# Performance work log

Hardware: AMD Instinct MI355X
Metric: run time of the kernel (lower is better)

## Reference

```python
import jax, jax.numpy as jnp
import numpy as np
import math

B, S, D, H, L, DFF, V = 4, 1024, 512, 8, 4, 2048, 32000
DK = D // H
SPARSITY = 0.3
K = max(1, int(S * SPARSITY))  # 307
EPS = 1e-5


def _layernorm(x, g, b):
    mu = jnp.mean(x, axis=-1, keepdims=True)
    var = jnp.mean(jnp.square(x - mu), axis=-1, keepdims=True)
    return (x - mu) * jax.lax.rsqrt(var + EPS) * g + b


def _scatter_topk(scores, k):
    # scores: [B,H,S,S]. keep top-k per row, others -inf (torch.topk + scatter_)
    vals, idx = jax.lax.top_k(scores, k)
    lead = int(np.prod(scores.shape[:-1]))
    sk = scores.shape[-1]
    sparse = jnp.full((lead, sk), -jnp.inf, dtype=scores.dtype)
    rows = jnp.arange(lead)[:, None]
    sparse = sparse.at[rows, idx.reshape(lead, k)].set(vals.reshape(lead, k))
    return sparse.reshape(scores.shape)


def _forward(x, tok_emb, pos_emb, Wq, bq, Wk, bk, Wv, bv, Wo, bo,
             g1, be1, g2, be2, W1, b1, Wm, bm, W2, b2, Wout, bout):
    h = tok_emb[x] + pos_emb[jnp.arange(S)][None, :, :]  # [B,S,D]
    scale = 1.0 / math.sqrt(DK)
    for l in range(L):
        y = _layernorm(h, g1[l], be1[l])
        q = (y @ Wq[l] + bq[l]).reshape(B, S, H, DK).transpose(0, 2, 1, 3)
        kk = (y @ Wk[l] + bk[l]).reshape(B, S, H, DK).transpose(0, 2, 1, 3)
        v = (y @ Wv[l] + bv[l]).reshape(B, S, H, DK).transpose(0, 2, 1, 3)
        scores = jnp.einsum('bhqd,bhkd->bhqk', q, kk) * scale
        sparse = _scatter_topk(scores, K)
        attn = jax.nn.softmax(sparse, axis=-1)
        o = jnp.einsum('bhqk,bhkd->bhqd', attn, v)
        o = o.transpose(0, 2, 1, 3).reshape(B, S, D) @ Wo[l] + bo[l]
        h = h + o
        z = _layernorm(h, g2[l], be2[l])
        f = jax.nn.gelu(z @ W1[l] + b1[l], approximate=False)
        f = jax.nn.gelu(f @ Wm[l] + bm[l], approximate=False)
        f = f @ W2[l] + b2[l]
        h = h + f
    return h @ Wout + bout  # logits [B,S,V]


def setup_inputs() -> dict:
    key = jax.random.key(0)
    ks = iter(jax.random.split(key, 32))
    xa = lambda shape, fan: (jax.random.normal(next(ks), shape, jnp.float32)
                             * math.sqrt(2.0 / fan))
    return {
        'x': jax.random.randint(next(ks), (B, S), 0, V, dtype=jnp.int32),
        'tok_emb': xa((V, D), V + D),
        'pos_emb': xa((S, D), S + D),
        'Wq': xa((L, D, D), 2 * D), 'bq': jnp.zeros((L, D), jnp.float32),
        'Wk': xa((L, D, D), 2 * D), 'bk': jnp.zeros((L, D), jnp.float32),
        'Wv': xa((L, D, D), 2 * D), 'bv': jnp.zeros((L, D), jnp.float32),
        'Wo': xa((L, D, D), 2 * D), 'bo': jnp.zeros((L, D), jnp.float32),
        'g1': jnp.ones((L, D), jnp.float32), 'be1': jnp.zeros((L, D), jnp.float32),
        'g2': jnp.ones((L, D), jnp.float32), 'be2': jnp.zeros((L, D), jnp.float32),
        'W1': xa((L, D, DFF), D + DFF), 'b1': jnp.zeros((L, DFF), jnp.float32),
        'Wm': xa((L, DFF, DFF), 2 * DFF), 'bm': jnp.zeros((L, DFF), jnp.float32),
        'W2': xa((L, DFF, D), D + DFF), 'b2': jnp.zeros((L, D), jnp.float32),
        'Wout': xa((D, V), D + V), 'bout': jnp.zeros((V,), jnp.float32),
    }


def reference(x, tok_emb, pos_emb, Wq, bq, Wk, bk, Wv, bv, Wo, bo,
              g1, be1, g2, be2, W1, b1, Wm, bm, W2, b2, Wout, bout):
    return _forward(x, tok_emb, pos_emb, Wq, bq, Wk, bk, Wv, bv, Wo, bo,
                    g1, be1, g2, be2, W1, b1, Wm, bm, W2, b2, Wout, bout)
```

## Files before the change

### kernel.cpp

```cpp
#include <hip/hip_runtime.h>
#include <hip/hip_bf16.h>
#include <math.h>

#define B_ 4
#define S_ 1024
#define D_ 512
#define H_ 8
#define L_ 4
#define DFF_ 2048
#define V_ 32000
#define DK_ 64
#define KTOP 307
#define SRS 1048

using bf16x8 = __attribute__((ext_vector_type(8))) __bf16;
using bf16x4 = __attribute__((ext_vector_type(4))) __bf16;
using bf16x2 = __attribute__((ext_vector_type(2))) __bf16;
using f32x4v = __attribute__((ext_vector_type(4))) float;

__device__ __forceinline__ void gload_lds16(const __bf16* g, __bf16* l) {
  __builtin_amdgcn_global_load_lds(
      (const __attribute__((address_space(1))) void*)g,
      (__attribute__((address_space(3))) void*)l, 16, 0, 0);
}

__device__ __forceinline__ unsigned int f32_to_bf16_bits(float s) {
  unsigned int x = __float_as_uint(s);
  return (x + 0x7FFFu + ((x >> 16) & 1u)) >> 16;
}

__global__ void embed_kernel(const int* __restrict__ x, const float* __restrict__ tok,
                             const float* __restrict__ pos, float* __restrict__ h) {
  int row = blockIdx.x;
  int t = threadIdx.x;
  int s = row & (S_ - 1);
  int token = x[row];
  const float4* t4 = reinterpret_cast<const float4*>(tok + (size_t)token * D_);
  const float4* p4 = reinterpret_cast<const float4*>(pos + (size_t)s * D_);
  float4 a = t4[t];
  float4 b = p4[t];
  a.x += b.x; a.y += b.y; a.z += b.z; a.w += b.w;
  reinterpret_cast<float4*>(h + (size_t)row * D_)[t] = a;
}

__global__ void ln_kernel(const float* __restrict__ xin, const float* __restrict__ g,
                          const float* __restrict__ bta, __bf16* __restrict__ y) {
  int row = blockIdx.x;
  int t = threadIdx.x;
  const float2* x2 = reinterpret_cast<const float2*>(xin + (size_t)row * D_);
  float2 v = x2[t];
  float s = v.x + v.y;
  #pragma unroll
  for (int m = 1; m < 64; m <<= 1) s += __shfl_xor(s, m, 64);
  __shared__ float red[4];
  __shared__ float red2[4];
  int wid = t >> 6, lane = t & 63;
  if (lane == 0) red[wid] = s;
  __syncthreads();
  float mu = (red[0] + red[1] + red[2] + red[3]) * (1.0f / D_);
  float dx = v.x - mu, dy = v.y - mu;
  float s2 = dx * dx + dy * dy;
  #pragma unroll
  for (int m = 1; m < 64; m <<= 1) s2 += __shfl_xor(s2, m, 64);
  if (lane == 0) red2[wid] = s2;
  __syncthreads();
  float var = (red2[0] + red2[1] + red2[2] + red2[3]) * (1.0f / D_);
  float rstd = rsqrtf(var + 1e-5f);
  float2 gg = reinterpret_cast<const float2*>(g)[t];
  float2 bb = reinterpret_cast<const float2*>(bta)[t];
  bf16x2 o2;
  o2[0] = (__bf16)(dx * rstd * gg.x + bb.x);
  o2[1] = (__bf16)(dy * rstd * gg.y + bb.y);
  *reinterpret_cast<bf16x2*>(y + (size_t)row * D_ + t * 2) = o2;
}

__global__ void transpose_bf16_kernel(const float* __restrict__ in, __bf16* __restrict__ out,
                                      int Kd, int N, long in_bstride, long out_bstride) {
  __shared__ float tile[32][33];
  const float* ib = in + (size_t)blockIdx.z * in_bstride;
  __bf16* ob = out + (size_t)blockIdx.z * out_bstride;
  int n0 = blockIdx.x * 32, k0 = blockIdx.y * 32;
  int tx = threadIdx.x & 31, ty = threadIdx.x >> 5;
  #pragma unroll
  for (int i = 0; i < 4; ++i)
    tile[ty + i * 8][tx] = ib[(size_t)(k0 + ty + i * 8) * N + n0 + tx];
  __syncthreads();
  #pragma unroll
  for (int i = 0; i < 4; ++i)
    ob[(size_t)(n0 + ty + i * 8) * Kd + k0 + tx] = (__bf16)tile[tx][ty + i * 8];
}

__global__ void concat_bias_kernel(const float* __restrict__ bq, const float* __restrict__ bk,
                                   const float* __restrict__ bv, float* __restrict__ bqkv) {
  int i = blockIdx.x * 256 + threadIdx.x;
  int l = i / 1536, c = i - l * 1536;
  float v = (c < 512) ? bq[l * 512 + c]
          : (c < 1024) ? bk[l * 512 + c - 512]
                       : bv[l * 512 + c - 1024];
  bqkv[i] = v;
}

#define BM 128
#define BN 128
#define BK 32

template<int OMODE, bool GELU_ACT, bool RES, bool SWZ>
__global__ __launch_bounds__(256)
void gemm_bf16_kernel(const __bf16* __restrict__ A, const __bf16* __restrict__ WT,
                      const float* __restrict__ bias, const float* __restrict__ res,
                      void* __restrict__ outp, void* __restrict__ outp2, void* __restrict__ outp3,
                      int M, int N, int Kd) {
  __shared__ __bf16 As[BM * BK];
  __shared__ __bf16 Ws[BN * BK];
  int tid = threadIdx.x;
  int lane = tid & 63, w = tid >> 6;
  int wr = w >> 1, wc = w & 1;
  int lr = lane & 15, lg = lane >> 4;
  int bx, by;
  if (SWZ) {
    int lid = blockIdx.x;
    int cpx = gridDim.x >> 3;
    int swz = (lid & 7) * cpx + (lid >> 3);
    int gx = M >> 7;
    bx = swz % gx;
    by = swz / gx;
  } else {
    bx = blockIdx.x; by = blockIdx.y;
  }
  int row0 = bx * BM, col0 = by * BN;

  int srow = lane >> 2;
  int schunk = lane & 3;
  const __bf16* Abase = A + (size_t)(row0 + srow) * Kd + schunk * 8;
  const __bf16* Wbase = WT + (size_t)(col0 + srow) * Kd + schunk * 8;

  f32x4v acc[4][4];
  #pragma unroll
  for (int i = 0; i < 4; ++i)
    #pragma unroll
    for (int j = 0; j < 4; ++j)
      #pragma unroll
      for (int e = 0; e < 4; ++e) acc[i][j][e] = 0.0f;

  for (int k0 = 0; k0 < Kd; k0 += BK) {
    #pragma unroll
    for (int p = 0; p < 2; ++p) {
      int r0 = p * 64 + w * 16;
      gload_lds16(Abase + (size_t)r0 * Kd + k0, &As[r0 * BK]);
      gload_lds16(Wbase + (size_t)r0 * Kd + k0, &Ws[r0 * BK]);
    }
    __syncthreads();
    bf16x8 af[4], bfr[4];
    #pragma unroll
    for (int mr = 0; mr < 4; ++mr)
      af[mr] = *reinterpret_cast<const bf16x8*>(&As[(wr * 64 + mr * 16 + lr) * BK + lg * 8]);
    #pragma unroll
    for (int nc = 0; nc < 4; ++nc)
      bfr[nc] = *reinterpret_cast<const bf16x8*>(&Ws[(wc * 64 + nc * 16 + lr) * BK + lg * 8]);
    #pragma unroll
    for (int mr = 0; mr < 4; ++mr)
      #pragma unroll
      for (int nc = 0; nc < 4; ++nc)
        acc[mr][nc] = __builtin_amdgcn_mfma_f32_16x16x32_bf16(af[mr], bfr[nc], acc[mr][nc], 0, 0, 0);
    __syncthreads();
  }

  #pragma unroll
  for (int mr = 0; mr < 4; ++mr) {
    #pragma unroll
    for (int nc = 0; nc < 4; ++nc) {
      int c = col0 + wc * 64 + nc * 16 + lr;
      int rb = row0 + wr * 64 + mr * 16 + lg * 4;
      float vv[4];
      #pragma unroll
      for (int j = 0; j < 4; ++j) {
        float t = acc[mr][nc][j] + bias[c];
        if (RES) t += res[(size_t)(rb + j) * N + c];
        if (GELU_ACT) t = 0.5f * t * (1.0f + erff(t * 0.70710678118654752f));
        vv[j] = t;
      }
      if (OMODE == 0) {
        float* out = (float*)outp;
        #pragma unroll
        for (int j = 0; j < 4; ++j) out[(size_t)(rb + j) * N + c] = vv[j];
      } else if (OMODE == 1) {
        __bf16* out = (__bf16*)outp;
        #pragma unroll
        for (int j = 0; j < 4; ++j) out[(size_t)(rb + j) * N + c] = (__bf16)vv[j];
      } else if (OMODE == 3) {
        float* out = (float*)outp;
        __bf16* out2 = (__bf16*)outp2;
        #pragma unroll
        for (int j = 0; j < 4; ++j) {
          out[(size_t)(rb + j) * N + c] = vv[j];
          out2[(size_t)(rb + j) * N + c] = (__bf16)vv[j];
        }
      } else {
        if (col0 < 512) {
          __bf16* out = (__bf16*)outp;
          #pragma unroll
          for (int j = 0; j < 4; ++j) out[(size_t)(rb + j) * D_ + c] = (__bf16)vv[j];
        } else if (col0 < 1024) {
          __bf16* out = (__bf16*)outp2;
          #pragma unroll
          for (int j = 0; j < 4; ++j) out[(size_t)(rb + j) * D_ + (c - 512)] = (__bf16)vv[j];
        } else {
          __bf16* out = (__bf16*)outp3;
          int b = rb >> 10, s0 = rb & (S_ - 1);
          bf16x4 pk;
          #pragma unroll
          for (int j = 0; j < 4; ++j) pk[j] = (__bf16)vv[j];
          *reinterpret_cast<bf16x4*>(&out[((size_t)b * D_ + (c - 1024)) * S_ + s0]) = pk;
        }
      }
    }
  }
}

template<int OMODE, bool RES>
__global__ __launch_bounds__(256)
void gemm64_kernel(const __bf16* __restrict__ A, const __bf16* __restrict__ WT,
                   const float* __restrict__ bias, const float* __restrict__ res,
                   void* __restrict__ outp, void* __restrict__ outp2,
                   int M, int N, int Kd) {
  __shared__ __bf16 As[64 * BK];
  __shared__ __bf16 Ws[BN * BK];
  int tid = threadIdx.x;
  int lane = tid & 63, w = tid >> 6;
  int wr = w >> 1, wc = w & 1;
  int lr = lane & 15, lg = lane >> 4;
  int row0 = blockIdx.x * 64, col0 = blockIdx.y * BN;

  int srow = lane >> 2;
  int schunk = lane & 3;
  const __bf16* Abase = A + (size_t)(row0 + srow) * Kd + schunk * 8;
  const __bf16* Wbase = WT + (size_t)(col0 + srow) * Kd + schunk * 8;

  f32x4v acc[2][4];
  #pragma unroll
  for (int i = 0; i < 2; ++i)
    #pragma unroll
    for (int j = 0; j < 4; ++j)
      #pragma unroll
      for (int e = 0; e < 4; ++e) acc[i][j][e] = 0.0f;

  for (int k0 = 0; k0 < Kd; k0 += BK) {
    gload_lds16(Abase + (size_t)(w * 16) * Kd + k0, &As[w * 16 * BK]);
    #pragma unroll
    for (int p = 0; p < 2; ++p) {
      int r0 = p * 64 + w * 16;
      gload_lds16(Wbase + (size_t)r0 * Kd + k0, &Ws[r0 * BK]);
    }
    __syncthreads();
    bf16x8 af[2], bfr[4];
    #pragma unroll
    for (int mr = 0; mr < 2; ++mr)
      af[mr] = *reinterpret_cast<const bf16x8*>(&As[(wr * 32 + mr * 16 + lr) * BK + lg * 8]);
    #pragma unroll
    for (int nc = 0; nc < 4; ++nc)
      bfr[nc] = *reinterpret_cast<const bf16x8*>(&Ws[(wc * 64 + nc * 16 + lr) * BK + lg * 8]);
    #pragma unroll
    for (int mr = 0; mr < 2; ++mr)
      #pragma unroll
      for (int nc = 0; nc < 4; ++nc)
        acc[mr][nc] = __builtin_amdgcn_mfma_f32_16x16x32_bf16(af[mr], bfr[nc], acc[mr][nc], 0, 0, 0);
    __syncthreads();
  }

  #pragma unroll
  for (int mr = 0; mr < 2; ++mr) {
    #pragma unroll
    for (int nc = 0; nc < 4; ++nc) {
      int c = col0 + wc * 64 + nc * 16 + lr;
      int rb = row0 + wr * 32 + mr * 16 + lg * 4;
      float vv[4];
      #pragma unroll
      for (int j = 0; j < 4; ++j) {
        float t = acc[mr][nc][j] + bias[c];
        if (RES) t += res[(size_t)(rb + j) * N + c];
        vv[j] = t;
      }
      if (OMODE == 0) {
        float* out = (float*)outp;
        #pragma unroll
        for (int j = 0; j < 4; ++j) out[(size_t)(rb + j) * N + c] = vv[j];
      } else {
        float* out = (float*)outp;
        __bf16* out2 = (__bf16*)outp2;
        #pragma unroll
        for (int j = 0; j < 4; ++j) {
          out[(size_t)(rb + j) * N + c] = vv[j];
          out2[(size_t)(rb + j) * N + c] = (__bf16)vv[j];
        }
      }
    }
  }
}

__global__ __launch_bounds__(256)
void attn_kernel(const __bf16* __restrict__ qm, const __bf16* __restrict__ km,
                 const __bf16* __restrict__ vt, __bf16* __restrict__ o) {
  __shared__ unsigned short sc16[16][SRS];
  __shared__ float rs[16];
  const int q0 = blockIdx.x * 16;
  const int hh = blockIdx.y;
  const int bb = blockIdx.z;
  const int tid = threadIdx.x;
  const int lane = tid & 63, w = tid >> 6;
  const int lr = lane & 15, lg = lane >> 4;

  const __bf16* qrow = qm + ((size_t)(bb * S_ + q0 + lr)) * D_ + hh * DK_;
  bf16x8 qf0 = *reinterpret_cast<const bf16x8*>(qrow + lg * 8);
  bf16x8 qf1 = *reinterpret_cast<const bf16x8*>(qrow + 32 + lg * 8);

  const __bf16* kbase = km + ((size_t)bb * S_) * D_ + hh * DK_;
  #pragma unroll 4
  for (int kt = 0; kt < 16; ++kt) {
    int key0 = kt * 64 + w * 16;
    const __bf16* krow = kbase + (size_t)(key0 + lr) * D_;
    bf16x8 kf0 = *reinterpret_cast<const bf16x8*>(krow + lg * 8);
    bf16x8 kf1 = *reinterpret_cast<const bf16x8*>(krow + 32 + lg * 8);
    f32x4v d = {0.0f, 0.0f, 0.0f, 0.0f};
    d = __builtin_amdgcn_mfma_f32_16x16x32_bf16(qf0, kf0, d, 0, 0, 0);
    d = __builtin_amdgcn_mfma_f32_16x16x32_bf16(qf1, kf1, d, 0, 0, 0);
    #pragma unroll
    for (int j = 0; j < 4; ++j) {
      unsigned int u = f32_to_bf16_bits(d[j] * 0.125f);
      u = (u & 0x8000u) ? (~u & 0xFFFFu) : (u | 0x8000u);
      sc16[lg * 4 + j][key0 + lr] = (unsigned short)u;
    }
  }
  __syncthreads();

  {
    int r = tid >> 4, tc = tid & 15;
    const unsigned int* srow = reinterpret_cast<const unsigned int*>(&sc16[r][0]);
    unsigned int wv[32];
    #pragma unroll
    for (int g = 0; g < 8; ++g) {
      uint4 t4 = *reinterpret_cast<const uint4*>(&srow[g * 64 + tc * 4]);
      wv[g * 4 + 0] = t4.x; wv[g * 4 + 1] = t4.y;
      wv[g * 4 + 2] = t4.z; wv[g * 4 + 3] = t4.w;
    }
    unsigned int umax = 0;
    #pragma unroll
    for (int i = 0; i < 32; ++i) {
      unsigned int a = wv[i] & 0xFFFFu, b = wv[i] >> 16;
      unsigned int mx = a > b ? a : b;
      umax = mx > umax ? mx : umax;
    }
    #pragma unroll
    for (int m = 1; m < 16; m <<= 1) {
      unsigned int other = (unsigned int)__shfl_xor((int)umax, m, 64);
      umax = other > umax ? other : umax;
    }
    unsigned int lo = 0;
    for (int bit = 15; bit >= 0; --bit) {
      unsigned int cs = (lo | (1u << bit)) << 16;
      int cnt = 0;
      #pragma unroll
      for (int i = 0; i < 32; ++i) {
        cnt += ((wv[i] << 16) >= cs) ? 1 : 0;
        cnt += (wv[i] >= cs) ? 1 : 0;
      }
      #pragma unroll
      for (int m = 1; m < 16; m <<= 1) cnt += __shfl_xor(cnt, m, 64);
      if (cnt >= KTOP) lo |= (1u << bit);
    }
    unsigned int um = (umax & 0x8000u) ? (umax ^ 0x8000u) : (~umax & 0xFFFFu);
    float mval = __uint_as_float(um << 16);

    __bf16* P = reinterpret_cast<__bf16*>(&sc16[r][0]);
    float lsum = 0.0f;
    #pragma unroll
    for (int g = 0; g < 8; ++g) {
      bf16x8 pk;
      #pragma unroll
      for (int e = 0; e < 8; ++e) {
        unsigned int wrd = wv[g * 4 + (e >> 1)];
        unsigned int u = (e & 1) ? (wrd >> 16) : (wrd & 0xFFFFu);
        float p = 0.0f;
        if (u >= lo) {
          unsigned int ub = (u & 0x8000u) ? (u ^ 0x8000u) : (~u & 0xFFFFu);
          p = __expf(__uint_as_float(ub << 16) - mval);
        }
        pk[e] = (__bf16)p;
        lsum += (float)pk[e];
      }
      *reinterpret_cast<bf16x8*>(&P[tc * 8 + g * 128]) = pk;
    }
    #pragma unroll
    for (int m = 1; m < 16; m <<= 1) lsum += __shfl_xor(lsum, m, 64);
    if (tc == 0) rs[r] = lsum;
  }
  __syncthreads();

  {
    const __bf16* P0 = reinterpret_cast<const __bf16*>(&sc16[0][0]);
    const __bf16* vbase = vt + ((size_t)bb * D_ + hh * DK_ + w * 16 + lr) * S_;
    const __bf16* prow = P0 + (size_t)lr * SRS;
    f32x4v oacc = {0.0f, 0.0f, 0.0f, 0.0f};
    #pragma unroll 4
    for (int kt = 0; kt < 32; ++kt) {
      bf16x8 a = *reinterpret_cast<const bf16x8*>(prow + kt * 32 + lg * 8);
      bf16x8 b = *reinterpret_cast<const bf16x8*>(vbase + kt * 32 + lg * 8);
      oacc = __builtin_amdgcn_mfma_f32_16x16x32_bf16(a, b, oacc, 0, 0, 0);
    }
    #pragma unroll
    for (int j = 0; j < 4; ++j) {
      int qr = lg * 4 + j;
      float ov = oacc[j] / rs[qr];
      o[((size_t)(bb * S_ + q0 + qr)) * D_ + hh * DK_ + w * 16 + lr] = (__bf16)ov;
    }
  }
}

extern "C" void kernel_launch(void* const* d_in, const int* in_sizes, int n_in,
                              void* d_out, int out_size, void* d_ws, size_t ws_size,
                              hipStream_t stream) {
  (void)in_sizes; (void)n_in; (void)out_size; (void)ws_size;
  const int*   x    = (const int*)d_in[0];
  const float* tok  = (const float*)d_in[1];
  const float* pos  = (const float*)d_in[2];
  const float* Wq   = (const float*)d_in[3];
  const float* bq   = (const float*)d_in[4];
  const float* Wk   = (const float*)d_in[5];
  const float* bk   = (const float*)d_in[6];
  const float* Wv   = (const float*)d_in[7];
  const float* bv   = (const float*)d_in[8];
  const float* Wo   = (const float*)d_in[9];
  const float* bo   = (const float*)d_in[10];
  const float* g1   = (const float*)d_in[11];
  const float* be1  = (const float*)d_in[12];
  const float* g2   = (const float*)d_in[13];
  const float* be2  = (const float*)d_in[14];
  const float* W1   = (const float*)d_in[15];
  const float* b1   = (const float*)d_in[16];
  const float* Wm   = (const float*)d_in[17];
  const float* bm   = (const float*)d_in[18];
  const float* W2   = (const float*)d_in[19];
  const float* b2   = (const float*)d_in[20];
  const float* Wout = (const float*)d_in[21];
  const float* bout = (const float*)d_in[22];
  float* logits = (float*)d_out;

  const int M = B_ * S_;
  float* ws = (float*)d_ws;
  float* h    = ws;
  float* bqkv = h + (size_t)M * D_;
  __bf16* y16  = (__bf16*)(bqkv + (size_t)L_ * 1536);
  __bf16* f1b  = y16  + (size_t)M * D_;
  __bf16* f2b  = f1b  + (size_t)M * DFF_;
  __bf16* qb16 = f2b  + (size_t)M * DFF_;
  __bf16* kb16 = qb16 + (size_t)M * D_;
  __bf16* vt16 = kb16 + (size_t)M * D_;
  __bf16* ob16 = vt16 + (size_t)M * D_;
  __bf16* h16  = ob16 + (size_t)M * D_;
  __bf16* WqkvT = h16 + (size_t)M * D_;
  __bf16* WoT  = WqkvT + (size_t)L_ * 1536 * D_;
  __bf16* W1T  = WoT  + (size_t)L_ * D_ * D_;
  __bf16* WmT  = W1T  + (size_t)L_ * D_ * DFF_;
  __bf16* W2T  = WmT  + (size_t)L_ * DFF_ * DFF_;
  __bf16* WoutT = W2T + (size_t)L_ * D_ * DFF_;

  const long DD = (long)D_ * D_;
  transpose_bf16_kernel<<<dim3(D_/32,  D_/32,   L_), 256, 0, stream>>>(Wq, WqkvT,            D_, D_, DD, 1536L*D_);
  transpose_bf16_kernel<<<dim3(D_/32,  D_/32,   L_), 256, 0, stream>>>(Wk, WqkvT + 512*512,  D_, D_, DD, 1536L*D_);
  transpose_bf16_kernel<<<dim3(D_/32,  D_/32,   L_), 256, 0, stream>>>(Wv, WqkvT + 1024*512, D_, D_, DD, 1536L*D_);
  transpose_bf16_kernel<<<dim3(D_/32,  D_/32,   L_), 256, 0, stream>>>(Wo, WoT, D_, D_, DD, DD);
  transpose_bf16_kernel<<<dim3(DFF_/32, D_/32,  L_), 256, 0, stream>>>(W1, W1T, D_, DFF_, (long)D_*DFF_, (long)D_*DFF_);
  transpose_bf16_kernel<<<dim3(DFF_/32, DFF_/32,L_), 256, 0, stream>>>(Wm, WmT, DFF_, DFF_, (long)DFF_*DFF_, (long)DFF_*DFF_);
  transpose_bf16_kernel<<<dim3(D_/32,  DFF_/32, L_), 256, 0, stream>>>(W2, W2T, DFF_, D_, (long)D_*DFF_, (long)D_*DFF_);
  transpose_bf16_kernel<<<dim3(V_/32,  D_/32,   1 ), 256, 0, stream>>>(Wout, WoutT, D_, V_, (long)D_*V_, (long)D_*V_);
  concat_bias_kernel<<<(L_*1536)/256, 256, 0, stream>>>(bq, bk, bv, bqkv);

  embed_kernel<<<M, 128, 0, stream>>>(x, tok, pos, h);

  for (int l = 0; l < L_; ++l) {
    ln_kernel<<<M, 256, 0, stream>>>(h, g1 + l * D_, be1 + l * D_, y16);
    gemm_bf16_kernel<4,false,false,false><<<dim3(M/BM, 1536/BN), 256, 0, stream>>>(
        y16, WqkvT + (size_t)l * 1536 * D_, bqkv + l * 1536, nullptr,
        qb16, kb16, vt16, M, 1536, D_);
    attn_kernel<<<dim3(S_/16, H_, B_), 256, 0, stream>>>(qb16, kb16, vt16, ob16);
    gemm64_kernel<0,true><<<dim3(M/64, D_/BN), 256, 0, stream>>>(
        ob16, WoT + (size_t)l * DD, bo + l * D_, h, h, nullptr, M, D_, D_);
    ln_kernel<<<M, 256, 0, stream>>>(h, g2 + l * D_, be2 + l * D_, y16);
    gemm_bf16_kernel<1,true,false,false><<<dim3(M/BM, DFF_/BN), 256, 0, stream>>>(
        y16, W1T + (size_t)l * D_ * DFF_, b1 + l * DFF_, nullptr, f1b, nullptr, nullptr, M, DFF_, D_);
    gemm_bf16_kernel<1,true,false,false><<<dim3(M/BM, DFF_/BN), 256, 0, stream>>>(
        f1b, WmT + (size_t)l * DFF_ * DFF_, bm + l * DFF_, nullptr, f2b, nullptr, nullptr, M, DFF_, DFF_);
    gemm64_kernel<3,true><<<dim3(M/64, D_/BN), 256, 0, stream>>>(
        f2b, W2T + (size_t)l * D_ * DFF_, b2 + l * D_, h, h, h16, M, D_, DFF_);
  }
  gemm_bf16_kernel<0,false,false,true><<<dim3((M/BM) * (V_/BN)), 256, 0, stream>>>(
      h16, WoutT, bout, nullptr, logits, nullptr, nullptr, M, V_, D_);
}
```

Baseline: 1.408 ms.

## Widen GEMM K-tile with swizzled LDS, add double-buffered 256x256 LM-head GEMM

BK goes from 32 to 64, and the tiles are staged through a helper that uses an XOR-swizzled LDS layout to cut bank conflicts. MFMA sections are raised in priority with s_setprio, and that is also applied in the attention kernel. The QKV and FFN GEMMs now use the swizzled block-to-tile mapping. The vocab projection moves to a new 512-thread kernel with 256x256 tiles and double-buffered LDS prefetch. The new head kernel uses 128KB of LDS and hand-written waitcnt ordering, which limits occupancy and is fragile if the schedule changes.

```diff
diff --git a/kernel.cpp b/kernel.cpp
--- a/kernel.cpp
+++ b/kernel.cpp
@@ -27,6 +27,34 @@
 __device__ __forceinline__ unsigned int f32_to_bf16_bits(float s) {
   unsigned int x = __float_as_uint(s);
   return (x + 0x7FFFu + ((x >> 16) & 1u)) >> 16;
+}
+
+template<int ROWS>
+__device__ __forceinline__ void stage_tile4(const __bf16* src, int Kd, __bf16* lds,
+                                            int w, int lane) {
+  #pragma unroll
+  for (int c = 0; c < ROWS / 32; ++c) {
+    int rblk = (c * 4 + w) * 8;
+    int row = rblk + (lane >> 3);
+    int col = (lane & 7) * 8;
+    int scol = col ^ ((row & 4) ? 16 : 0);
+    gload_lds16(src + (size_t)row * Kd + scol, lds + rblk * 64);
+  }
+}
+__device__ __forceinline__ void stage_half8(const __bf16* src, int Kd, __bf16* lds,
+                                            int w, int lane) {
+  #pragma unroll
+  for (int c = 0; c < 2; ++c) {
+    int rblk = (c * 8 + w) * 8;
+    int row = rblk + (lane >> 3);
+    int col = (lane & 7) * 8;
+    int scol = col ^ ((row & 4) ? 16 : 0);
+    gload_lds16(src + (size_t)row * Kd + scol, lds + rblk * 64);
+  }
+}
+__device__ __forceinline__ bf16x8 lds_frag64(const __bf16* lds, int row, int colbase) {
+  int col = colbase ^ ((row & 4) ? 16 : 0);
+  return *reinterpret_cast<const bf16x8*>(lds + row * 64 + col);
 }
 
 __global__ void embed_kernel(const int* __restrict__ x, const float* __restrict__ tok,
@@ -102,7 +130,7 @@
 
 #define BM 128
 #define BN 128
-#define BK 32
+#define BK 64
 
 template<int OMODE, bool GELU_ACT, bool RES, bool SWZ>
 __global__ __launch_bounds__(256)
@@ -129,10 +157,8 @@
   }
   int row0 = bx * BM, col0 = by * BN;
 
-  int srow = lane >> 2;
-  int schunk = lane & 3;
-  const __bf16* Abase = A + (size_t)(row0 + srow) * Kd + schunk * 8;
-  const __bf16* Wbase = WT + (size_t)(col0 + srow) * Kd + schunk * 8;
+  const __bf16* Abase = A + (size_t)row0 * Kd;
+  const __bf16* Wbase = WT + (size_t)col0 * Kd;
 
   f32x4v acc[4][4];
   #pragma unroll
@@ -143,25 +169,29 @@
       for (int e = 0; e < 4; ++e) acc[i][j][e] = 0.0f;
 
   for (int k0 = 0; k0 < Kd; k0 += BK) {
-    #pragma unroll
-    for (int p = 0; p < 2; ++p) {
-      int r0 = p * 64 + w * 16;
-      gload_lds16(Abase + (size_t)r0 * Kd + k0, &As[r0 * BK]);
-      gload_lds16(Wbase + (size_t)r0 * Kd + k0, &Ws[r0 * BK]);
-    }
+    stage_tile4<128>(Abase + k0, Kd, As, w, lane);
+    stage_tile4<128>(Wbase + k0, Kd, Ws, w, lane);
     __syncthreads();
-    bf16x8 af[4], bfr[4];
+    bf16x8 af[4][2], bfr[4][2];
     #pragma unroll
     for (int mr = 0; mr < 4; ++mr)
-      af[mr] = *reinterpret_cast<const bf16x8*>(&As[(wr * 64 + mr * 16 + lr) * BK + lg * 8]);
+      #pragma unroll
+      for (int kk = 0; kk < 2; ++kk)
+        af[mr][kk] = lds_frag64(As, wr * 64 + mr * 16 + lr, kk * 32 + lg * 8);
     #pragma unroll
     for (int nc = 0; nc < 4; ++nc)
-      bfr[nc] = *reinterpret_cast<const bf16x8*>(&Ws[(wc * 64 + nc * 16 + lr) * BK + lg * 8]);
+      #pragma unroll
+      for (int kk = 0; kk < 2; ++kk)
+        bfr[nc][kk] = lds_frag64(Ws, wc * 64 + nc * 16 + lr, kk * 32 + lg * 8);
+    __builtin_amdgcn_s_setprio(1);
     #pragma unroll
     for (int mr = 0; mr < 4; ++mr)
       #pragma unroll
-      for (int nc = 0; nc < 4; ++nc)
-        acc[mr][nc] = __builtin_amdgcn_mfma_f32_16x16x32_bf16(af[mr], bfr[nc], acc[mr][nc], 0, 0, 0);
+      for (int nc = 0; nc < 4; ++nc) {
+        acc[mr][nc] = __builtin_amdgcn_mfma_f32_16x16x32_bf16(af[mr][0], bfr[nc][0], acc[mr][nc], 0, 0, 0);
+        acc[mr][nc] = __builtin_amdgcn_mfma_f32_16x16x32_bf16(af[mr][1], bfr[nc][1], acc[mr][nc], 0, 0, 0);
+      }
+    __builtin_amdgcn_s_setprio(0);
     __syncthreads();
   }
 
@@ -231,10 +261,8 @@
   int lr = lane & 15, lg = lane >> 4;
   int row0 = blockIdx.x * 64, col0 = blockIdx.y * BN;
 
-  int srow = lane >> 2;
-  int schunk = lane & 3;
-  const __bf16* Abase = A + (size_t)(row0 + srow) * Kd + schunk * 8;
-  const __bf16* Wbase = WT + (size_t)(col0 + srow) * Kd + schunk * 8;
+  const __bf16* Abase = A + (size_t)row0 * Kd;
+  const __bf16* Wbase = WT + (size_t)col0 * Kd;
 
   f32x4v acc[2][4];
   #pragma unroll
@@ -245,25 +273,29 @@
       for (int e = 0; e < 4; ++e) acc[i][j][e] = 0.0f;
 
   for (int k0 = 0; k0 < Kd; k0 += BK) {
-    gload_lds16(Abase + (size_t)(w * 16) * Kd + k0, &As[w * 16 * BK]);
-    #pragma unroll
-    for (int p = 0; p < 2; ++p) {
-      int r0 = p * 64 + w * 16;
-      gload_lds16(Wbase + (size_t)r0 * Kd + k0, &Ws[r0 * BK]);
-    }
+    stage_tile4<64>(Abase + k0, Kd, As, w, lane);
+    stage_tile4<128>(Wbase + k0, Kd, Ws, w, lane);
     __syncthreads();
-    bf16x8 af[2], bfr[4];
+    bf16x8 af[2][2], bfr[4][2];
     #pragma unroll
     for (int mr = 0; mr < 2; ++mr)
-      af[mr] = *reinterpret_cast<const bf16x8*>(&As[(wr * 32 + mr * 16 + lr) * BK + lg * 8]);
+      #pragma unroll
+      for (int kk = 0; kk < 2; ++kk)
+        af[mr][kk] = lds_frag64(As, wr * 32 + mr * 16 + lr, kk * 32 + lg * 8);
     #pragma unroll
     for (int nc = 0; nc < 4; ++nc)
-      bfr[nc] = *reinterpret_cast<const bf16x8*>(&Ws[(wc * 64 + nc * 16 + lr) * BK + lg * 8]);
+      #pragma unroll
+      for (int kk = 0; kk < 2; ++kk)
+        bfr[nc][kk] = lds_frag64(Ws, wc * 64 + nc * 16 + lr, kk * 32 + lg * 8);
+    __builtin_amdgcn_s_setprio(1);
     #pragma unroll
     for (int mr = 0; mr < 2; ++mr)
       #pragma unroll
-      for (int nc = 0; nc < 4; ++nc)
-        acc[mr][nc] = __builtin_amdgcn_mfma_f32_16x16x32_bf16(af[mr], bfr[nc], acc[mr][nc], 0, 0, 0);
+      for (int nc = 0; nc < 4; ++nc) {
+        acc[mr][nc] = __builtin_amdgcn_mfma_f32_16x16x32_bf16(af[mr][0], bfr[nc][0], acc[mr][nc], 0, 0, 0);
+        acc[mr][nc] = __builtin_amdgcn_mfma_f32_16x16x32_bf16(af[mr][1], bfr[nc][1], acc[mr][nc], 0, 0, 0);
+      }
+    __builtin_amdgcn_s_setprio(0);
     __syncthreads();
   }
 
@@ -293,6 +325,102 @@
           out2[(size_t)(rb + j) * N + c] = (__bf16)vv[j];
         }
       }
+    }
+  }
+}
+
+__global__ __launch_bounds__(512)
+void gemm_head_kernel(const __bf16* __restrict__ A, const __bf16* __restrict__ WT,
+                      const float* __restrict__ bias, float* __restrict__ out,
+                      int M, int N, int Kd) {
+  __shared__ __bf16 lds[2][2][256 * 64];
+  const int tid = threadIdx.x;
+  const int lane = tid & 63, w = tid >> 6;
+  const int wr = w >> 2, wc = w & 3;
+  const int lr = lane & 15, lg = lane >> 4;
+
+  int lid = blockIdx.x;
+  int cpx = gridDim.x >> 3;
+  int swz = (lid & 7) * cpx + (lid >> 3);
+  int gx = M >> 8;
+  int bx = swz % gx, by = swz / gx;
+  int row0 = bx * 256, col0 = by * 256;
+
+  const __bf16* Asrc = A + (size_t)row0 * Kd;
+  const __bf16* Bsrc = WT + (size_t)col0 * Kd;
+
+  f32x4v acc[8][4];
+  #pragma unroll
+  for (int i = 0; i < 8; ++i)
+    #pragma unroll
+    for (int j = 0; j < 4; ++j)
+      #pragma unroll
+      for (int e = 0; e < 4; ++e) acc[i][j][e] = 0.0f;
+
+  const int NT = Kd / 64;
+  stage_half8(Asrc,                      Kd, &lds[0][0][0],    w, lane);
+  stage_half8(Asrc + (size_t)128 * Kd,   Kd, &lds[0][0][8192], w, lane);
+  stage_half8(Bsrc,                      Kd, &lds[0][1][0],    w, lane);
+  stage_half8(Bsrc + (size_t)128 * Kd,   Kd, &lds[0][1][8192], w, lane);
+
+  for (int t = 0; t < NT; ++t) {
+    int cur = t & 1, nxt = cur ^ 1;
+    int k1 = (t + 1) * 64;
+    const __bf16* Ab = &lds[cur][0][0];
+    const __bf16* Bb = &lds[cur][1][0];
+    bf16x8 bfr[4][2];
+    #pragma unroll
+    for (int p = 0; p < 4; ++p) {
+      if (t < NT - 1) {
+        const __bf16* s;
+        __bf16* d;
+        if (p == 0)      { s = Asrc + k1;                    d = &lds[nxt][0][0]; }
+        else if (p == 1) { s = Asrc + (size_t)128 * Kd + k1; d = &lds[nxt][0][8192]; }
+        else if (p == 2) { s = Bsrc + k1;                    d = &lds[nxt][1][0]; }
+        else             { s = Bsrc + (size_t)128 * Kd + k1; d = &lds[nxt][1][8192]; }
+        stage_half8(s, Kd, d, w, lane);
+      }
+      if (p == 0) {
+        if (t < NT - 1) asm volatile("s_waitcnt vmcnt(2)" ::: "memory");
+        else            asm volatile("s_waitcnt vmcnt(0)" ::: "memory");
+        __builtin_amdgcn_s_barrier();
+        #pragma unroll
+        for (int nn = 0; nn < 4; ++nn)
+          #pragma unroll
+          for (int kk = 0; kk < 2; ++kk)
+            bfr[nn][kk] = lds_frag64(Bb, wc * 64 + nn * 16 + lr, kk * 32 + lg * 8);
+      }
+      bf16x8 af[2][2];
+      #pragma unroll
+      for (int mm = 0; mm < 2; ++mm)
+        #pragma unroll
+        for (int kk = 0; kk < 2; ++kk)
+          af[mm][kk] = lds_frag64(Ab, wr * 128 + p * 32 + mm * 16 + lr, kk * 32 + lg * 8);
+      asm volatile("s_waitcnt lgkmcnt(0)" ::: "memory");
+      __builtin_amdgcn_sched_barrier(0);
+      __builtin_amdgcn_s_setprio(1);
+      #pragma unroll
+      for (int mm = 0; mm < 2; ++mm)
+        #pragma unroll
+        for (int nn = 0; nn < 4; ++nn) {
+          acc[p * 2 + mm][nn] = __builtin_amdgcn_mfma_f32_16x16x32_bf16(af[mm][0], bfr[nn][0], acc[p * 2 + mm][nn], 0, 0, 0);
+          acc[p * 2 + mm][nn] = __builtin_amdgcn_mfma_f32_16x16x32_bf16(af[mm][1], bfr[nn][1], acc[p * 2 + mm][nn], 0, 0, 0);
+        }
+      __builtin_amdgcn_s_setprio(0);
+    }
+    __builtin_amdgcn_s_barrier();
+  }
+
+  #pragma unroll
+  for (int mg = 0; mg < 8; ++mg) {
+    #pragma unroll
+    for (int nn = 0; nn < 4; ++nn) {
+      int c = col0 + wc * 64 + nn * 16 + lr;
+      int rb = row0 + wr * 128 + mg * 16 + lg * 4;
+      float b = bias[c];
+      #pragma unroll
+      for (int j = 0; j < 4; ++j)
+        out[(size_t)(rb + j) * N + c] = acc[mg][nn][j] + b;
     }
   }
 }
@@ -321,8 +449,10 @@
     bf16x8 kf0 = *reinterpret_cast<const bf16x8*>(krow + lg * 8);
     bf16x8 kf1 = *reinterpret_cast<const bf16x8*>(krow + 32 + lg * 8);
     f32x4v d = {0.0f, 0.0f, 0.0f, 0.0f};
+    __builtin_amdgcn_s_setprio(1);
     d = __builtin_amdgcn_mfma_f32_16x16x32_bf16(qf0, kf0, d, 0, 0, 0);
     d = __builtin_amdgcn_mfma_f32_16x16x32_bf16(qf1, kf1, d, 0, 0, 0);
+    __builtin_amdgcn_s_setprio(0);
     #pragma unroll
     for (int j = 0; j < 4; ++j) {
       unsigned int u = f32_to_bf16_bits(d[j] * 0.125f);
@@ -404,7 +534,9 @@
     for (int kt = 0; kt < 32; ++kt) {
       bf16x8 a = *reinterpret_cast<const bf16x8*>(prow + kt * 32 + lg * 8);
       bf16x8 b = *reinterpret_cast<const bf16x8*>(vbase + kt * 32 + lg * 8);
+      __builtin_amdgcn_s_setprio(1);
       oacc = __builtin_amdgcn_mfma_f32_16x16x32_bf16(a, b, oacc, 0, 0, 0);
+      __builtin_amdgcn_s_setprio(0);
     }
     #pragma unroll
     for (int j = 0; j < 4; ++j) {
@@ -478,20 +610,20 @@
 
   for (int l = 0; l < L_; ++l) {
     ln_kernel<<<M, 256, 0, stream>>>(h, g1 + l * D_, be1 + l * D_, y16);
-    gemm_bf16_kernel<4,false,false,false><<<dim3(M/BM, 1536/BN), 256, 0, stream>>>(
+    gemm_bf16_kernel<4,false,false,true><<<dim3((M/BM) * (1536/BN)), 256, 0, stream>>>(
         y16, WqkvT + (size_t)l * 1536 * D_, bqkv + l * 1536, nullptr,
         qb16, kb16, vt16, M, 1536, D_);
     attn_kernel<<<dim3(S_/16, H_, B_), 256, 0, stream>>>(qb16, kb16, vt16, ob16);
     gemm64_kernel<0,true><<<dim3(M/64, D_/BN), 256, 0, stream>>>(
         ob16, WoT + (size_t)l * DD, bo + l * D_, h, h, nullptr, M, D_, D_);
     ln_kernel<<<M, 256, 0, stream>>>(h, g2 + l * D_, be2 + l * D_, y16);
-    gemm_bf16_kernel<1,true,false,false><<<dim3(M/BM, DFF_/BN), 256, 0, stream>>>(
+    gemm_bf16_kernel<1,true,false,true><<<dim3((M/BM) * (DFF_/BN)), 256, 0, stream>>>(
         y16, W1T + (size_t)l * D_ * DFF_, b1 + l * DFF_, nullptr, f1b, nullptr, nullptr, M, DFF_, D_);
-    gemm_bf16_kernel<1,true,false,false><<<dim3(M/BM, DFF_/BN), 256, 0, stream>>>(
+    gemm_bf16_kernel<1,true,false,true><<<dim3((M/BM) * (DFF_/BN)), 256, 0, stream>>>(
         f1b, WmT + (size_t)l * DFF_ * DFF_, bm + l * DFF_, nullptr, f2b, nullptr, nullptr, M, DFF_, DFF_);
     gemm64_kernel<3,true><<<dim3(M/64, D_/BN), 256, 0, stream>>>(
         f2b, W2T + (size_t)l * D_ * DFF_, b2 + l * D_, h, h, h16, M, D_, DFF_);
   }
-  gemm_bf16_kernel<0,false,false,true><<<dim3((M/BM) * (V_/BN)), 256, 0, stream>>>(
-      h16, WoutT, bout, nullptr, logits, nullptr, nullptr, M, V_, D_);
-}
+  gemm_head_kernel<<<dim3((M/256) * (V_/256)), 512, 0, stream>>>(
+      h16, WoutT, bout, logits, M, V_, D_);
+}
```

New measurement: 1.344 ms. -4.5%, faster.
